# Performance work log

Measured on AMD Instinct MI355X. Metric: run time of the kernel, lower is better.

Reference implementation:

```python
import jax, jax.numpy as jnp
import numpy as np

SPATIAL = ((100, 100), (50, 50), (25, 25), (13, 13))  # (h, w) per level
D_MODEL, H, L, P = 256, 8, 4, 4
HD = D_MODEL // H


def setup_inputs() -> dict:
    key = jax.random.key(0)
    ks = jax.random.split(key, 12)
    B = 2
    Lv = sum(h * w for h, w in SPATIAL)  # 13294
    Lq = Lv
    s = 0.02
    return {
        'query': jax.random.normal(ks[0], (B, Lq, D_MODEL), jnp.float32),
        'reference_points': jax.random.uniform(ks[1], (B, Lq, L, 2), jnp.float32),
        'value': jax.random.normal(ks[2], (B, Lv, D_MODEL), jnp.float32),
        'spatial_shapes': jnp.array(SPATIAL, jnp.int32),
        'W_off': jax.random.normal(ks[3], (D_MODEL, H * L * P * 2), jnp.float32) * s,
        'b_off': jax.random.normal(ks[4], (H * L * P * 2,), jnp.float32) * s,
        'W_attn': jax.random.normal(ks[5], (D_MODEL, H * L * P), jnp.float32) * s,
        'b_attn': jax.random.normal(ks[6], (H * L * P,), jnp.float32) * s,
        'W_v': jax.random.normal(ks[7], (D_MODEL, D_MODEL), jnp.float32) * s,
        'b_v': jax.random.normal(ks[8], (D_MODEL,), jnp.float32) * s,
        'W_out': jax.random.normal(ks[9], (D_MODEL, D_MODEL), jnp.float32) * s,
        'b_out': jax.random.normal(ks[10], (D_MODEL,), jnp.float32) * s,
    }


def _grid_sample_zeros(v, grid, h, w):
    # v: [N, HD, h*w] flattened feature map; grid: [N, Q, P, 2] in [-1, 1]
    # torch grid_sample bilinear, align_corners=False, padding_mode='zeros'
    x = (grid[..., 0] + 1.0) * (w * 0.5) - 0.5
    y = (grid[..., 1] + 1.0) * (h * 0.5) - 0.5
    x0 = jnp.floor(x); y0 = jnp.floor(y)
    x1 = x0 + 1.0;     y1 = y0 + 1.0
    wx1 = x - x0; wx0 = 1.0 - wx1
    wy1 = y - y0; wy0 = 1.0 - wy1

    def gather(xi, yi, wgt):
        valid = (xi >= 0) & (xi < w) & (yi >= 0) & (yi < h)
        xc = jnp.clip(xi, 0, w - 1).astype(jnp.int32)
        yc = jnp.clip(yi, 0, h - 1).astype(jnp.int32)
        idx = yc * w + xc                       # [N, Q, P]
        N, Q, Pp = idx.shape
        g = jnp.take_along_axis(v, idx.reshape(N, 1, Q * Pp), axis=2)
        g = g.reshape(N, v.shape[1], Q, Pp)     # [N, HD, Q, P]
        return g * (wgt * valid)[:, None, :, :]

    return (gather(x0, y0, wx0 * wy0) + gather(x1, y0, wx1 * wy0) +
            gather(x0, y1, wx0 * wy1) + gather(x1, y1, wx1 * wy1))


def reference(query, reference_points, value, spatial_shapes,
              W_off, b_off, W_attn, b_attn, W_v, b_v, W_out, b_out):
    B, Lq, _ = query.shape
    Lv = value.shape[1]
    v = (value @ W_v + b_v).reshape(B, Lv, H, HD)
    off = (query @ W_off + b_off).reshape(B, Lq, H, L, P, 2)
    aw = jax.nn.softmax((query @ W_attn + b_attn).reshape(B, Lq, H, L * P), axis=-1)
    # normalize offsets by (w, h) per level, add to reference points
    wh = jnp.array([[w_, h_] for h_, w_ in SPATIAL], jnp.float32)   # [L, 2]
    loc = reference_points[:, :, None, :, None, :] + off / wh[None, None, None, :, None, :]
    grids = 2.0 * loc - 1.0                                          # [B, Lq, H, L, P, 2]

    sampled = []
    start = 0
    for lid, (h_, w_) in enumerate(SPATIAL):
        n = h_ * w_
        vl = v[:, start:start + n].transpose(0, 2, 3, 1).reshape(B * H, HD, n)
        gl = grids[:, :, :, lid].transpose(0, 2, 1, 3, 4).reshape(B * H, Lq, P, 2)
        sampled.append(_grid_sample_zeros(vl, gl, h_, w_))           # [B*H, HD, Lq, P]
        start += n
    sv = jnp.concatenate(sampled, axis=-1)                           # [B*H, HD, Lq, L*P]
    awr = aw.transpose(0, 2, 1, 3).reshape(B * H, 1, Lq, L * P)
    out = (sv * awr).sum(-1)                                         # [B*H, HD, Lq]
    out = out.reshape(B, H, HD, Lq).transpose(0, 3, 1, 2).reshape(B, Lq, D_MODEL)
    return out @ W_out + b_out
```

## Files before the change

### kernel.cpp

```cpp
#include <hip/hip_runtime.h>
#include <hip/hip_bf16.h>
#include <math.h>


namespace {
constexpr int LQ    = 13294;
constexpr int LV    = 13294;
constexpr int NROWS = 2 * LQ;
}

typedef __attribute__((ext_vector_type(8))) short short8;
typedef __attribute__((ext_vector_type(4))) float f32x4;

__device__ inline float bf2f(unsigned u16) {
    union { unsigned u; float f; } c; c.u = u16 << 16; return c.f;
}
__device__ inline unsigned short f2bf(float f) {
    __hip_bfloat16 h = __float2bfloat16(f);
    return *reinterpret_cast<unsigned short*>(&h);
}

__global__ __launch_bounds__(256) void prep_weights(
    const float* __restrict__ Wv, const float* __restrict__ Woff,
    const float* __restrict__ Wattn, const float* __restrict__ Wout,
    __hip_bfloat16* __restrict__ WTf)
{
    const int c = blockIdx.x, k = threadIdx.x;
    float v;
    if (c < 256)      v = Wv[k * 256 + c];
    else if (c < 512) v = Woff[k * 256 + (c - 256)];
    else if (c < 640) v = Wattn[k * 128 + (c - 512)];
    else              v = Wout[k * 256 + (c - 640)];
    const int lane = (c & 15) | (((k >> 3) & 3) << 4);
    const size_t dst = ((size_t)((c >> 4) * 8 + (k >> 5)) * 64 + lane) * 8 + (k & 7);
    WTf[dst] = __float2bfloat16(v);
}

template<int NT, int OUTMODE, bool A_FP32>
__device__ __forceinline__ void gemm_core(
    short (*As)[264], const void* __restrict__ Xv,
    const __hip_bfloat16* __restrict__ WTf, int ct0,
    const float* __restrict__ bias, void* __restrict__ Yv,
    int ldY, int coloff, int M, int bx)
{
    const int t  = threadIdx.x;
    const int r0 = bx * 64;

    if (A_FP32) {
        const float* X = (const float*)Xv;
        #pragma unroll
        for (int i = 0; i < 16; ++i) {
            const int f4 = i * 256 + t;
            int row = r0 + (f4 >> 6);
            if (row >= M) row = M - 1;
            const int col4 = f4 & 63;
            const float4 u = *(const float4*)(X + (size_t)row * 256 + col4 * 4);
            union { unsigned short us[4]; uint2 v; } p;
            p.us[0] = f2bf(u.x); p.us[1] = f2bf(u.y);
            p.us[2] = f2bf(u.z); p.us[3] = f2bf(u.w);
            *(uint2*)(&As[f4 >> 6][col4 * 4]) = p.v;
        }
    } else {
        const __hip_bfloat16* X = (const __hip_bfloat16*)Xv;
        #pragma unroll
        for (int i = 0; i < 8; ++i) {
            const int f8 = i * 256 + t;
            int row = r0 + (f8 >> 5);
            if (row >= M) row = M - 1;
            const int c16 = f8 & 31;
            *(short8*)(&As[f8 >> 5][c16 * 8]) =
                *(const short8*)(X + (size_t)row * 256 + c16 * 8);
        }
    }
    __syncthreads();

    const int lane = t & 63;
    const int wv   = t >> 6;
    const int r16  = lane & 15;
    const int koff = (lane >> 4) * 8;

    f32x4 acc[4][NT];
    #pragma unroll
    for (int rt = 0; rt < 4; ++rt)
        #pragma unroll
        for (int nt = 0; nt < NT; ++nt)
            #pragma unroll
            for (int j = 0; j < 4; ++j) acc[rt][nt][j] = 0.f;

    #pragma unroll
    for (int kc = 0; kc < 8; ++kc) {
        short8 a[4];
        #pragma unroll
        for (int rt = 0; rt < 4; ++rt)
            a[rt] = *(const short8*)(&As[rt * 16 + r16][kc * 32 + koff]);
        #pragma unroll
        for (int nt = 0; nt < NT; ++nt) {
            const int ct = ct0 + wv * NT + nt;
            const short8 bfr =
                *(const short8*)(WTf + ((size_t)(ct * 8 + kc) * 64 + lane) * 8);
            #pragma unroll
            for (int rt = 0; rt < 4; ++rt)
                acc[rt][nt] = __builtin_amdgcn_mfma_f32_16x16x32_bf16(
                    a[rt], bfr, acc[rt][nt], 0, 0, 0);
        }
    }

    const int orow = (lane >> 4) * 4;
    #pragma unroll
    for (int rt = 0; rt < 4; ++rt)
    #pragma unroll
    for (int nt = 0; nt < NT; ++nt) {
        const int lcol = wv * (NT * 16) + nt * 16 + r16;
        const float bb = bias[lcol];
        #pragma unroll
        for (int j = 0; j < 4; ++j) {
            const int rr = r0 + rt * 16 + orow + j;
            if (rr < M) {
                const float v = acc[rt][nt][j] + bb;
                if (OUTMODE == 0) {
                    ((float*)Yv)[(size_t)rr * ldY + coloff + lcol] = v;
                } else if (OUTMODE == 1) {
                    ((__hip_bfloat16*)Yv)[(size_t)rr * ldY + coloff + lcol] =
                        __float2bfloat16(v);
                } else {
                    const int b  = (rr >= LQ) ? 1 : 0;
                    const int lv = rr - b * LQ;
                    const int h  = lcol >> 5, cc = lcol & 31;
                    ((__hip_bfloat16*)Yv)[(((size_t)(b * 8 + h)) * LV + lv) * 32 + cc] =
                        __float2bfloat16(v);
                }
            }
        }
    }
}

__global__ __launch_bounds__(256, 2) void gemm_vq(
    const float* __restrict__ value, const float* __restrict__ query,
    const __hip_bfloat16* __restrict__ WTf,
    const float* __restrict__ bv, const float* __restrict__ boff,
    const float* __restrict__ battn,
    __hip_bfloat16* __restrict__ vhm, __hip_bfloat16* __restrict__ offlog, int M)
{
    __shared__ short As[64][264];
    if (blockIdx.y == 0)
        gemm_core<4, 2, true>(As, value, WTf, 0,  bv,    vhm,    0,   0,   M, blockIdx.x);
    else if (blockIdx.y == 1)
        gemm_core<4, 1, true>(As, query, WTf, 16, boff,  offlog, 384, 0,   M, blockIdx.x);
    else
        gemm_core<2, 1, true>(As, query, WTf, 32, battn, offlog, 384, 256, M, blockIdx.x);
}

__global__ __launch_bounds__(256, 2) void gemm_out_k(
    const __hip_bfloat16* __restrict__ sampled, const __hip_bfloat16* __restrict__ WTf,
    const float* __restrict__ bout, float* __restrict__ out, int M)
{
    __shared__ short As[64][264];
    gemm_core<4, 0, false>(As, sampled, WTf, 40, bout, out, 256, 0, M, blockIdx.x);
}

__global__ __launch_bounds__(256) void ms_sample(
    const __hip_bfloat16* __restrict__ vhm, const __hip_bfloat16* __restrict__ offlog,
    const float* __restrict__ refpts, __hip_bfloat16* __restrict__ sampled)
{
    __shared__ char params[4][16][304];

    const int t    = threadIdx.x;
    const int row0 = blockIdx.x * 4;

    #pragma unroll
    for (int it = 0; it < 2; ++it) {
        const int sid = it * 256 + t;
        const int rl  = sid >> 7;
        const int h   = (sid >> 4) & 7;
        const int s   = sid & 15;
        const int row = row0 + rl;
        const int l   = s >> 2;
        const int wl  = (l == 0) ? 100 : (l == 1) ? 50 : (l == 2) ? 25 : 13;
        const int st  = (l == 0) ? 0 : (l == 1) ? 10000 : (l == 2) ? 12500 : 13125;
        const float wlf = (float)wl;

        const unsigned short* ol = (const unsigned short*)offlog + (size_t)row * 384;
        const unsigned uoff = *(const unsigned*)(ol + h * 32 + s * 2);
        const float ox = bf2f(uoff & 0xffffu), oy = bf2f(uoff >> 16);
        const float lg = bf2f(ol[256 + h * 16 + s]);
        const float2 rf = *(const float2*)(refpts + (size_t)row * 8 + l * 2);

        float m = lg;
        #pragma unroll
        for (int o = 8; o > 0; o >>= 1) m = fmaxf(m, __shfl_xor(m, o, 16));
        const float e = __expf(lg - m);
        float ssum = e;
        #pragma unroll
        for (int o = 8; o > 0; o >>= 1) ssum += __shfl_xor(ssum, o, 16);
        const float a = e / ssum;

        const float x = fmaf(rf.x, wlf, ox) - 0.5f;
        const float y = fmaf(rf.y, wlf, oy) - 0.5f;
        const float x0f = floorf(x), y0f = floorf(y);
        const int   x0 = (int)x0f, y0 = (int)y0f;
        const float wx1 = x - x0f, wx0 = 1.f - wx1;
        const float wy1 = y - y0f, wy0 = 1.f - wy1;
        const bool xv0 = (unsigned)x0       < (unsigned)wl;
        const bool xv1 = (unsigned)(x0 + 1) < (unsigned)wl;
        const bool yv0 = (unsigned)y0       < (unsigned)wl;
        const bool yv1 = (unsigned)(y0 + 1) < (unsigned)wl;
        const float ax0 = a * wx0, ax1 = a * wx1;
        float w00 = ax0 * wy0, w10 = ax1 * wy0;
        float w01 = ax0 * wy1, w11 = ax1 * wy1;
        w00 = (xv0 && yv0) ? w00 : 0.f;
        w10 = (xv1 && yv0) ? w10 : 0.f;
        w01 = (xv0 && yv1) ? w01 : 0.f;
        w11 = (xv1 && yv1) ? w11 : 0.f;
        const int cx0 = min(max(x0, 0), wl - 1);
        const int cx1 = min(max(x0 + 1, 0), wl - 1);
        const int cy0 = min(max(y0, 0), wl - 1);
        const int cy1 = min(max(y0 + 1, 0), wl - 1);
        const int r0b = (st + cy0 * wl) * 64;
        const int r1b = (st + cy1 * wl) * 64;
        uint4  offs; offs.x = r0b + cx0 * 64; offs.y = r0b + cx1 * 64;
                     offs.z = r1b + cx0 * 64; offs.w = r1b + cx1 * 64;
        float4 wv4;  wv4.x = w00; wv4.y = w10; wv4.z = w01; wv4.w = w11;
        char* pe = &params[rl][s][h * 32];
        *(uint4*)pe         = offs;
        *(float4*)(pe + 16) = wv4;
    }
    __syncthreads();

    const int rl  = t >> 6;
    const int h   = (t >> 3) & 7;
    const int c4  = t & 7;
    const int row = row0 + rl;
    const int b   = (row >= LQ) ? 1 : 0;
    const char* vbase = (const char*)vhm + ((size_t)((b << 3) + h) * LV) * 64 + c4 * 8;

    float a0 = 0.f, a1 = 0.f, a2 = 0.f, a3 = 0.f;

    #pragma unroll
    for (int sq = 0; sq < 4; ++sq) {
        uint4  of[4]; float4 w[4];
        #pragma unroll
        for (int i = 0; i < 4; ++i) {
            const char* pe = &params[rl][sq * 4 + i][h * 32];
            of[i] = *(const uint4*)pe;
            w[i]  = *(const float4*)(pe + 16);
        }
        uint2 q0[4], q1[4], q2[4], q3[4];
        #pragma unroll
        for (int i = 0; i < 4; ++i) {
            q0[i] = *(const uint2*)(vbase + of[i].x);
            q1[i] = *(const uint2*)(vbase + of[i].y);
            q2[i] = *(const uint2*)(vbase + of[i].z);
            q3[i] = *(const uint2*)(vbase + of[i].w);
        }
        #pragma unroll
        for (int i = 0; i < 4; ++i) {
            union { unsigned u; float f; } lo, hi;
            lo.u = q0[i].x << 16;          a0 = fmaf(lo.f, w[i].x, a0);
            hi.u = q0[i].x & 0xffff0000u;  a1 = fmaf(hi.f, w[i].x, a1);
            lo.u = q0[i].y << 16;          a2 = fmaf(lo.f, w[i].x, a2);
            hi.u = q0[i].y & 0xffff0000u;  a3 = fmaf(hi.f, w[i].x, a3);
            lo.u = q1[i].x << 16;          a0 = fmaf(lo.f, w[i].y, a0);
            hi.u = q1[i].x & 0xffff0000u;  a1 = fmaf(hi.f, w[i].y, a1);
            lo.u = q1[i].y << 16;          a2 = fmaf(lo.f, w[i].y, a2);
            hi.u = q1[i].y & 0xffff0000u;  a3 = fmaf(hi.f, w[i].y, a3);
            lo.u = q2[i].x << 16;          a0 = fmaf(lo.f, w[i].z, a0);
            hi.u = q2[i].x & 0xffff0000u;  a1 = fmaf(hi.f, w[i].z, a1);
            lo.u = q2[i].y << 16;          a2 = fmaf(lo.f, w[i].z, a2);
            hi.u = q2[i].y & 0xffff0000u;  a3 = fmaf(hi.f, w[i].z, a3);
            lo.u = q3[i].x << 16;          a0 = fmaf(lo.f, w[i].w, a0);
            hi.u = q3[i].x & 0xffff0000u;  a1 = fmaf(hi.f, w[i].w, a1);
            lo.u = q3[i].y << 16;          a2 = fmaf(lo.f, w[i].w, a2);
            hi.u = q3[i].y & 0xffff0000u;  a3 = fmaf(hi.f, w[i].w, a3);
        }
    }

    uint2 o;
    o.x = (unsigned)f2bf(a0) | ((unsigned)f2bf(a1) << 16);
    o.y = (unsigned)f2bf(a2) | ((unsigned)f2bf(a3) << 16);
    *(uint2*)((unsigned short*)sampled + (size_t)row * 256 + h * 32 + c4 * 4) = o;
}

extern "C" void kernel_launch(void* const* d_in, const int* in_sizes, int n_in,
                              void* d_out, int out_size, void* d_ws, size_t ws_size,
                              hipStream_t stream)
{
    const float* query  = (const float*)d_in[0];
    const float* refpts = (const float*)d_in[1];
    const float* value  = (const float*)d_in[2];
    const float* Woff   = (const float*)d_in[4];
    const float* boff   = (const float*)d_in[5];
    const float* Wattn  = (const float*)d_in[6];
    const float* battn  = (const float*)d_in[7];
    const float* Wv     = (const float*)d_in[8];
    const float* bv     = (const float*)d_in[9];
    const float* Wout   = (const float*)d_in[10];
    const float* bout   = (const float*)d_in[11];
    float* out = (float*)d_out;

    constexpr size_t SZ_VHM = (size_t)2 * 8 * LV * 32;
    constexpr size_t SZ_OFF = (size_t)NROWS * 384;
    constexpr size_t SZ_ROW = (size_t)NROWS * 256;
    __hip_bfloat16* ws      = (__hip_bfloat16*)d_ws;
    __hip_bfloat16* vhm     = ws;
    __hip_bfloat16* offlog  = vhm + SZ_VHM;
    __hip_bfloat16* sampled = offlog + SZ_OFF;
    __hip_bfloat16* WTf     = sampled + SZ_ROW;

    const int gblk = (NROWS + 63) / 64;
    const int sblk = NROWS / 4;

    hipLaunchKernelGGL(prep_weights, dim3(896), dim3(256), 0, stream,
                       Wv, Woff, Wattn, Wout, WTf);
    hipLaunchKernelGGL(gemm_vq, dim3(gblk, 3), dim3(256), 0, stream,
                       value, query, WTf, bv, boff, battn, vhm, offlog, NROWS);
    hipLaunchKernelGGL(ms_sample, dim3(sblk), dim3(256), 0, stream,
                       vhm, offlog, refpts, sampled);
    hipLaunchKernelGGL(gemm_out_k, dim3(gblk), dim3(256), 0, stream,
                       sampled, WTf, bout, out, NROWS);
}
```

Measured before the change: 112.3 us.

## Split value GEMM from query GEMM, merge offset/attn projections, store value in fp16

Replaces the 3-way gemm_vq launch with a separate value-projection kernel and a single query kernel that computes offset and attention logits together (NT=6 with a split bias). The query tile is now converted and staged once instead of twice. The projected value tensor is stored as fp16 instead of bf16, and the sampler converts with half-to-float intrinsics. This adds one extra kernel launch, and the NT=6 kernel uses more registers. fp16 storage changes numerics, giving more mantissa bits but less range.

```diff
diff --git a/kernel.cpp b/kernel.cpp
--- a/kernel.cpp
+++ b/kernel.cpp
@@ -1,5 +1,6 @@
 #include <hip/hip_runtime.h>
 #include <hip/hip_bf16.h>
+#include <hip/hip_fp16.h>
 #include <math.h>
 
 
@@ -40,8 +41,8 @@
 __device__ __forceinline__ void gemm_core(
     short (*As)[264], const void* __restrict__ Xv,
     const __hip_bfloat16* __restrict__ WTf, int ct0,
-    const float* __restrict__ bias, void* __restrict__ Yv,
-    int ldY, int coloff, int M, int bx)
+    const float* __restrict__ biasA, const float* __restrict__ biasB, int bsplit,
+    void* __restrict__ Yv, int ldY, int M, int bx)
 {
     const int t  = threadIdx.x;
     const int r0 = bx * 64;
@@ -111,43 +112,45 @@
     #pragma unroll
     for (int nt = 0; nt < NT; ++nt) {
         const int lcol = wv * (NT * 16) + nt * 16 + r16;
-        const float bb = bias[lcol];
+        const float bb = (lcol < bsplit) ? biasA[lcol] : biasB[lcol - bsplit];
         #pragma unroll
         for (int j = 0; j < 4; ++j) {
             const int rr = r0 + rt * 16 + orow + j;
             if (rr < M) {
                 const float v = acc[rt][nt][j] + bb;
                 if (OUTMODE == 0) {
-                    ((float*)Yv)[(size_t)rr * ldY + coloff + lcol] = v;
+                    ((float*)Yv)[(size_t)rr * ldY + lcol] = v;
                 } else if (OUTMODE == 1) {
-                    ((__hip_bfloat16*)Yv)[(size_t)rr * ldY + coloff + lcol] =
+                    ((__hip_bfloat16*)Yv)[(size_t)rr * ldY + lcol] =
                         __float2bfloat16(v);
                 } else {
                     const int b  = (rr >= LQ) ? 1 : 0;
                     const int lv = rr - b * LQ;
                     const int h  = lcol >> 5, cc = lcol & 31;
-                    ((__hip_bfloat16*)Yv)[(((size_t)(b * 8 + h)) * LV + lv) * 32 + cc] =
-                        __float2bfloat16(v);
+                    ((__half*)Yv)[(((size_t)(b * 8 + h)) * LV + lv) * 32 + cc] =
+                        __float2half(v);
                 }
             }
         }
     }
 }
 
-__global__ __launch_bounds__(256, 2) void gemm_vq(
-    const float* __restrict__ value, const float* __restrict__ query,
-    const __hip_bfloat16* __restrict__ WTf,
-    const float* __restrict__ bv, const float* __restrict__ boff,
-    const float* __restrict__ battn,
-    __hip_bfloat16* __restrict__ vhm, __hip_bfloat16* __restrict__ offlog, int M)
+__global__ __launch_bounds__(256, 2) void gemm_v(
+    const float* __restrict__ value, const __hip_bfloat16* __restrict__ WTf,
+    const float* __restrict__ bv, __half* __restrict__ vhm, int M)
 {
     __shared__ short As[64][264];
-    if (blockIdx.y == 0)
-        gemm_core<4, 2, true>(As, value, WTf, 0,  bv,    vhm,    0,   0,   M, blockIdx.x);
-    else if (blockIdx.y == 1)
-        gemm_core<4, 1, true>(As, query, WTf, 16, boff,  offlog, 384, 0,   M, blockIdx.x);
-    else
-        gemm_core<2, 1, true>(As, query, WTf, 32, battn, offlog, 384, 256, M, blockIdx.x);
+    gemm_core<4, 2, true>(As, value, WTf, 0, bv, bv, 256, vhm, 0, M, blockIdx.x);
+}
+
+__global__ __launch_bounds__(256) void gemm_oq(
+    const float* __restrict__ query, const __hip_bfloat16* __restrict__ WTf,
+    const float* __restrict__ boff, const float* __restrict__ battn,
+    __hip_bfloat16* __restrict__ offlog, int M)
+{
+    __shared__ short As[64][264];
+    gemm_core<6, 1, true>(As, query, WTf, 16, boff, battn, 256, offlog, 384, M,
+                          blockIdx.x);
 }
 
 __global__ __launch_bounds__(256, 2) void gemm_out_k(
@@ -155,11 +158,12 @@
     const float* __restrict__ bout, float* __restrict__ out, int M)
 {
     __shared__ short As[64][264];
-    gemm_core<4, 0, false>(As, sampled, WTf, 40, bout, out, 256, 0, M, blockIdx.x);
+    gemm_core<4, 0, false>(As, sampled, WTf, 40, bout, bout, 256, out, 256, M,
+                           blockIdx.x);
 }
 
 __global__ __launch_bounds__(256) void ms_sample(
-    const __hip_bfloat16* __restrict__ vhm, const __hip_bfloat16* __restrict__ offlog,
+    const __half* __restrict__ vhm, const __hip_bfloat16* __restrict__ offlog,
     const float* __restrict__ refpts, __hip_bfloat16* __restrict__ sampled)
 {
     __shared__ char params[4][16][304];
@@ -254,23 +258,27 @@
         }
         #pragma unroll
         for (int i = 0; i < 4; ++i) {
-            union { unsigned u; float f; } lo, hi;
-            lo.u = q0[i].x << 16;          a0 = fmaf(lo.f, w[i].x, a0);
-            hi.u = q0[i].x & 0xffff0000u;  a1 = fmaf(hi.f, w[i].x, a1);
-            lo.u = q0[i].y << 16;          a2 = fmaf(lo.f, w[i].x, a2);
-            hi.u = q0[i].y & 0xffff0000u;  a3 = fmaf(hi.f, w[i].x, a3);
-            lo.u = q1[i].x << 16;          a0 = fmaf(lo.f, w[i].y, a0);
-            hi.u = q1[i].x & 0xffff0000u;  a1 = fmaf(hi.f, w[i].y, a1);
-            lo.u = q1[i].y << 16;          a2 = fmaf(lo.f, w[i].y, a2);
-            hi.u = q1[i].y & 0xffff0000u;  a3 = fmaf(hi.f, w[i].y, a3);
-            lo.u = q2[i].x << 16;          a0 = fmaf(lo.f, w[i].z, a0);
-            hi.u = q2[i].x & 0xffff0000u;  a1 = fmaf(hi.f, w[i].z, a1);
-            lo.u = q2[i].y << 16;          a2 = fmaf(lo.f, w[i].z, a2);
-            hi.u = q2[i].y & 0xffff0000u;  a3 = fmaf(hi.f, w[i].z, a3);
-            lo.u = q3[i].x << 16;          a0 = fmaf(lo.f, w[i].w, a0);
-            hi.u = q3[i].x & 0xffff0000u;  a1 = fmaf(hi.f, w[i].w, a1);
-            lo.u = q3[i].y << 16;          a2 = fmaf(lo.f, w[i].w, a2);
-            hi.u = q3[i].y & 0xffff0000u;  a3 = fmaf(hi.f, w[i].w, a3);
+            union { unsigned u; __half2 h2; } c0, c1;
+            c0.u = q0[i].x; c1.u = q0[i].y;
+            a0 = fmaf(__low2float(c0.h2),  w[i].x, a0);
+            a1 = fmaf(__high2float(c0.h2), w[i].x, a1);
+            a2 = fmaf(__low2float(c1.h2),  w[i].x, a2);
+            a3 = fmaf(__high2float(c1.h2), w[i].x, a3);
+            c0.u = q1[i].x; c1.u = q1[i].y;
+            a0 = fmaf(__low2float(c0.h2),  w[i].y, a0);
+            a1 = fmaf(__high2float(c0.h2), w[i].y, a1);
+            a2 = fmaf(__low2float(c1.h2),  w[i].y, a2);
+            a3 = fmaf(__high2float(c1.h2), w[i].y, a3);
+            c0.u = q2[i].x; c1.u = q2[i].y;
+            a0 = fmaf(__low2float(c0.h2),  w[i].z, a0);
+            a1 = fmaf(__high2float(c0.h2), w[i].z, a1);
+            a2 = fmaf(__low2float(c1.h2),  w[i].z, a2);
+            a3 = fmaf(__high2float(c1.h2), w[i].z, a3);
+            c0.u = q3[i].x; c1.u = q3[i].y;
+            a0 = fmaf(__low2float(c0.h2),  w[i].w, a0);
+            a1 = fmaf(__high2float(c0.h2), w[i].w, a1);
+            a2 = fmaf(__low2float(c1.h2),  w[i].w, a2);
+            a3 = fmaf(__high2float(c1.h2), w[i].w, a3);
         }
     }
 
@@ -301,8 +309,8 @@
     constexpr size_t SZ_OFF = (size_t)NROWS * 384;
     constexpr size_t SZ_ROW = (size_t)NROWS * 256;
     __hip_bfloat16* ws      = (__hip_bfloat16*)d_ws;
-    __hip_bfloat16* vhm     = ws;
-    __hip_bfloat16* offlog  = vhm + SZ_VHM;
+    __half*         vhm     = (__half*)ws;
+    __hip_bfloat16* offlog  = ws + SZ_VHM;
     __hip_bfloat16* sampled = offlog + SZ_OFF;
     __hip_bfloat16* WTf     = sampled + SZ_ROW;
 
@@ -311,8 +319,10 @@
 
     hipLaunchKernelGGL(prep_weights, dim3(896), dim3(256), 0, stream,
                        Wv, Woff, Wattn, Wout, WTf);
-    hipLaunchKernelGGL(gemm_vq, dim3(gblk, 3), dim3(256), 0, stream,
-                       value, query, WTf, bv, boff, battn, vhm, offlog, NROWS);
+    hipLaunchKernelGGL(gemm_v, dim3(gblk), dim3(256), 0, stream,
+                       value, WTf, bv, vhm, NROWS);
+    hipLaunchKernelGGL(gemm_oq, dim3(gblk), dim3(256), 0, stream,
+                       query, WTf, boff, battn, offlog, NROWS);
     hipLaunchKernelGGL(ms_sample, dim3(sblk), dim3(256), 0, stream,
                        vhm, offlog, refpts, sampled);
     hipLaunchKernelGGL(gemm_out_k, dim3(gblk), dim3(256), 0, stream,
```

Result: slower. 124.4 us (+10.8%).
